# Performance work log

Hardware: AMD Instinct MI355X
Metric: run time of the kernel (lower is better)

The kernel has to match this reference:

```python
import jax, jax.numpy as jnp
import numpy as np

N = 100000   # nodes
E = 300000   # edges
D = 256      # emb_dim
FD = 512     # feat_dim
L = 5        # num_layer
G = 4000     # num graphs
NUM_ATOM = 100
NUM_BOND = 2
EPS = 1e-5


def setup_inputs() -> dict:
    key = jax.random.key(0)
    ks = jax.random.split(key, 24)
    s = 0.02
    inp = {
        "atomics": jax.random.randint(ks[0], (N,), 0, NUM_ATOM, dtype=jnp.int32),
        "pos": jax.random.normal(ks[1], (N, 3), dtype=jnp.float32),
        "edge_index": jax.random.randint(ks[2], (2, E), 0, N, dtype=jnp.int32),
        "edge_attr": jax.random.randint(ks[3], (E,), 0, NUM_BOND, dtype=jnp.int32),
        "batch": jnp.sort(jax.random.randint(ks[4], (N,), 0, G, dtype=jnp.int32)),
        # parameters
        "x_emb1": jax.random.normal(ks[5], (NUM_ATOM, D)) * s,
        "x_emb2_w": jax.random.normal(ks[6], (3, D)) * s,
        "x_emb2_b": jnp.zeros((D,), jnp.float32),
        "edge_emb": jax.random.normal(ks[7], (L, NUM_BOND, D)) * s,
        "mlp_w1": jax.random.normal(ks[8], (L, D, 2 * D)) * s,
        "mlp_b1": jnp.zeros((L, 2 * D), jnp.float32),
        "mlp_w2": jax.random.normal(ks[9], (L, 2 * D, D)) * s,
        "mlp_b2": jnp.zeros((L, D), jnp.float32),
        "bn_gamma": jnp.ones((L, D), jnp.float32),
        "bn_beta": jnp.zeros((L, D), jnp.float32),
        "feat_w": jax.random.normal(ks[10], (D, FD)) * s,
        "feat_b": jnp.zeros((FD,), jnp.float32),
        "head_w1": jax.random.normal(ks[11], (FD, FD // 2)) * s,
        "head_b1": jnp.zeros((FD // 2,), jnp.float32),
        "head_w2": jax.random.normal(ks[12], (FD // 2, 1)) * s,
        "head_b2": jnp.zeros((1,), jnp.float32),
    }
    return inp


def reference(atomics, pos, edge_index, edge_attr, batch,
              x_emb1, x_emb2_w, x_emb2_b, edge_emb,
              mlp_w1, mlp_b1, mlp_w2, mlp_b2, bn_gamma, bn_beta,
              feat_w, feat_b, head_w1, head_b1, head_w2, head_b2):
    n = atomics.shape[0]
    # initial node features: atom-type embedding + linear(pos)
    h = x_emb1[atomics] + pos @ x_emb2_w + x_emb2_b
    # add self loops (self-loop bond type = NUM_BOND-1)
    loop = jnp.arange(n, dtype=edge_index.dtype)
    src = jnp.concatenate([edge_index[0], loop])           # x_j (source)
    dst = jnp.concatenate([edge_index[1], loop])           # aggregate target
    eattr = jnp.concatenate([edge_attr,
                             jnp.full((n,), NUM_BOND - 1, dtype=edge_attr.dtype)])
    for l in range(L):
        msg = h[src] + edge_emb[l][eattr]                  # [E+N, D]
        agg = jax.ops.segment_sum(msg, dst, num_segments=n)
        # GINEConv MLP: Linear -> Softplus -> Linear
        h = jax.nn.softplus(agg @ mlp_w1[l] + mlp_b1[l]) @ mlp_w2[l] + mlp_b2[l]
        # BatchNorm1d (training mode: batch statistics, biased var)
        mean = h.mean(axis=0)
        var = h.var(axis=0)
        h = (h - mean) / jnp.sqrt(var + EPS) * bn_gamma[l] + bn_beta[l]
        if l < L - 1:
            h = jax.nn.softplus(h)
        # dropout with drop_ratio=0 is a no-op
    feat = h @ feat_w + feat_b                             # [N, FD]
    # global mean pool over graphs
    ssum = jax.ops.segment_sum(feat, batch, num_segments=G)
    cnt = jax.ops.segment_sum(jnp.ones((n,), feat.dtype), batch, num_segments=G)
    gfeat = ssum / jnp.maximum(cnt, 1.0)[:, None]          # [G, FD]
    hid = jax.nn.softplus(gfeat @ head_w1 + head_b1)
    return hid @ head_w2 + head_b2                          # [G, 1]
```

## Files before the change

kernel.cpp:

```cpp
#include <hip/hip_runtime.h>
#include <hip/hip_bf16.h>
#include <hip/hip_fp16.h>
#include <stdint.h>

#define D_  256
#define FD_ 512
#define L_  5
#define EPS_ 1e-5f

#define PLANE_SH 1056
#define TILE_SH  4224

typedef unsigned short ushort_t;
typedef __attribute__((ext_vector_type(8))) _Float16 h8v;
typedef __attribute__((ext_vector_type(4))) float    f4v;

__device__ __forceinline__ float sp(float x) {
    float t = __expf(-fabsf(x));
    return fmaxf(x, 0.f) + __logf(1.f + t);
}

__device__ __forceinline__ ushort_t f2h_bits(float v) {
    union { _Float16 h; ushort_t u; } c;
    c.h = (_Float16)v;
    return c.u;
}

__device__ __forceinline__ float h2f(ushort_t u) {
    union { ushort_t u; _Float16 h; } c;
    c.u = u;
    return (float)c.h;
}

__device__ __forceinline__ uint32_t pk2(float a, float b) {
    return (uint32_t)f2h_bits(a) | ((uint32_t)f2h_bits(b) << 16);
}

__device__ __forceinline__ size_t pk_off(int gm, int gn, int nKB) {
    return ((size_t)(gm >> 7) * nKB + (gn >> 5)) * TILE_SH
         + (size_t)((gn >> 3) & 3) * PLANE_SH
         + (gm & 127) * 8 + (gn & 7);
}

__global__ __launch_bounds__(256)
void init_h_kernel(const int* __restrict__ atomics, const float* __restrict__ pos,
                   const float* __restrict__ emb1, const float* __restrict__ w2,
                   const float* __restrict__ b2, ushort_t* __restrict__ h16, int N)
{
    int i = blockIdx.x;
    int d = threadIdx.x;
    int a = atomics[i];
    float p0 = pos[(size_t)i * 3 + 0];
    float p1 = pos[(size_t)i * 3 + 1];
    float p2 = pos[(size_t)i * 3 + 2];
    float v = emb1[(size_t)a * D_ + d]
            + p0 * w2[0 * D_ + d]
            + p1 * w2[1 * D_ + d]
            + p2 * w2[2 * D_ + d]
            + b2[d];
    h16[(size_t)i * D_ + d] = f2h_bits(v);
}

__global__ __launch_bounds__(256)
void hist_kernel(const int* __restrict__ dst, int* __restrict__ cnt, int E)
{
    int e = blockIdx.x * 256 + threadIdx.x;
    if (e < E) atomicAdd(&cnt[dst[e]], 1);
}

__global__ __launch_bounds__(256)
void alloc_kernel(const int* __restrict__ cnt, int* __restrict__ start,
                  int* __restrict__ cursor, int* __restrict__ total, int N)
{
    int i = blockIdx.x * 256 + threadIdx.x;
    if (i < N) {
        int s = atomicAdd(total, cnt[i]);
        start[i] = s;
        cursor[i] = s;
    }
}

__global__ __launch_bounds__(256)
void fill_kernel(const int* __restrict__ src, const int* __restrict__ dst,
                 const int* __restrict__ attr, int* __restrict__ cursor,
                 uint32_t* __restrict__ elist, int E)
{
    int e = blockIdx.x * 256 + threadIdx.x;
    if (e < E) {
        int p = atomicAdd(&cursor[dst[e]], 1);
        elist[p] = (uint32_t)src[e] | ((uint32_t)attr[e] << 30);
    }
}

__global__ __launch_bounds__(256)
void range_kernel(const int* __restrict__ batch, int* __restrict__ gstart,
                  int* __restrict__ gend, int N)
{
    int i = blockIdx.x * 256 + threadIdx.x;
    if (i >= N) return;
    int b = batch[i];
    if (i == 0 || batch[i - 1] != b) gstart[b] = i;
    if (i == N - 1 || batch[i + 1] != b) gend[b] = i + 1;
}

__global__ __launch_bounds__(256)
void act16_kernel(const ushort_t* __restrict__ h16, ushort_t* __restrict__ hact,
                  const float* __restrict__ bnsum, const float* __restrict__ gamma,
                  const float* __restrict__ beta, long long total16, float invN)
{
    __shared__ float ssc[256], ssh[256];
    int t = threadIdx.x;
    {
        float mean = bnsum[t] * invN;
        float var = bnsum[D_ + t] * invN - mean * mean;
        float sc = gamma[t] * rsqrtf(fmaxf(var, 0.f) + EPS_);
        ssc[t] = sc;
        ssh[t] = beta[t] - mean * sc;
    }
    __syncthreads();
    long long idx = (long long)blockIdx.x * 256 + t;
    if (idx >= total16) return;
    int c0 = (int)((idx * 16) & 255);
    uint4 in0 = *(const uint4*)(h16 + idx * 16);
    uint4 in1 = *(const uint4*)(h16 + idx * 16 + 8);
    ushort_t* ip0 = (ushort_t*)&in0;
    ushort_t* ip1 = (ushort_t*)&in1;
    ushort_t ov[16];
#pragma unroll
    for (int j = 0; j < 8; ++j)
        ov[j] = f2h_bits(sp(h2f(ip0[j]) * ssc[c0 + j] + ssh[c0 + j]));
#pragma unroll
    for (int j = 0; j < 8; ++j)
        ov[8 + j] = f2h_bits(sp(h2f(ip1[j]) * ssc[c0 + 8 + j] + ssh[c0 + 8 + j]));
    *(uint4*)(hact + idx * 16)     = *(uint4*)&ov[0];
    *(uint4*)(hact + idx * 16 + 8) = *(uint4*)&ov[8];
}

__global__ __launch_bounds__(256)
void gather2_kernel(const ushort_t* __restrict__ hact, const uint32_t* __restrict__ elist,
                    const int* __restrict__ start, const int* __restrict__ cnt,
                    const float* __restrict__ ee_l, ushort_t* __restrict__ aggP, int N)
{
    int t = threadIdx.x;
    int d0 = (t & 127) * 2;
    int ib = __builtin_amdgcn_readfirstlane(blockIdx.x * 8 + (t >> 7) * 4);
    float2 e0 = *(const float2*)(ee_l + d0);
    float2 e1 = *(const float2*)(ee_l + D_ + d0);
    int sbase[4], sdeg[4];
    float ax[4], ay[4];
    int mdeg = 0;
#pragma unroll
    for (int r = 0; r < 4; ++r) {
        int i = ib + r;
        sbase[r] = 0; sdeg[r] = 0; ax[r] = 0.f; ay[r] = 0.f;
        if (i < N) {
            sbase[r] = start[i];
            sdeg[r]  = cnt[i];
            uint32_t hv = *(const uint32_t*)(hact + (size_t)i * D_ + d0);
            ax[r] = h2f((ushort_t)hv) + e1.x;
            ay[r] = h2f((ushort_t)(hv >> 16)) + e1.y;
            mdeg = (sdeg[r] > mdeg) ? sdeg[r] : mdeg;
        }
    }
    for (int j = 0; j < mdeg; j += 2) {
        uint32_t pA[4], pB[4];
#pragma unroll
        for (int r = 0; r < 4; ++r) {
            pA[r] = elist[(j     < sdeg[r]) ? sbase[r] + j     : 0];
            pB[r] = elist[(j + 1 < sdeg[r]) ? sbase[r] + j + 1 : 0];
        }
        uint32_t hvA[4], hvB[4];
#pragma unroll
        for (int r = 0; r < 4; ++r)
            hvA[r] = *(const uint32_t*)(hact + (size_t)(pA[r] & 0x3FFFFFFF) * D_ + d0);
#pragma unroll
        for (int r = 0; r < 4; ++r)
            hvB[r] = *(const uint32_t*)(hact + (size_t)(pB[r] & 0x3FFFFFFF) * D_ + d0);
#pragma unroll
        for (int r = 0; r < 4; ++r) {
            if (j < sdeg[r]) {
                bool b1 = (pA[r] >> 30) != 0;
                ax[r] += h2f((ushort_t)hvA[r]) + (b1 ? e1.x : e0.x);
                ay[r] += h2f((ushort_t)(hvA[r] >> 16)) + (b1 ? e1.y : e0.y);
            }
            if (j + 1 < sdeg[r]) {
                bool b1 = (pB[r] >> 30) != 0;
                ax[r] += h2f((ushort_t)hvB[r]) + (b1 ? e1.x : e0.x);
                ay[r] += h2f((ushort_t)(hvB[r] >> 16)) + (b1 ? e1.y : e0.y);
            }
        }
    }
#pragma unroll
    for (int r = 0; r < 4; ++r) {
        int i = ib + r;
        if (i < N) {
            size_t o = pk_off(i, d0, 8);
            *(uint32_t*)(aggP + o) = pk2(ax[r], ay[r]);
        }
    }
}

__global__ __launch_bounds__(256)
void pool_bn_kernel(const ushort_t* __restrict__ h16, const float* __restrict__ bnsum,
                    const float* __restrict__ gamma, const float* __restrict__ beta,
                    const int* __restrict__ gstart, const int* __restrict__ gend,
                    ushort_t* __restrict__ poolP, float invN)
{
    int g = blockIdx.x;
    int d = threadIdx.x;
    float mean = bnsum[d] * invN;
    float var = bnsum[D_ + d] * invN - mean * mean;
    float sc = gamma[d] * rsqrtf(fmaxf(var, 0.f) + EPS_);
    float sh = beta[d] - mean * sc;
    int s0 = gstart[g], s1 = gend[g];
    float acc = 0.f;
    int i = s0;
    for (; i + 4 <= s1; i += 4) {
        float a0 = h2f(h16[(size_t)(i + 0) * D_ + d]);
        float a1 = h2f(h16[(size_t)(i + 1) * D_ + d]);
        float a2 = h2f(h16[(size_t)(i + 2) * D_ + d]);
        float a3 = h2f(h16[(size_t)(i + 3) * D_ + d]);
        acc += (a0 + a1) + (a2 + a3);
    }
    for (; i < s1; ++i)
        acc += h2f(h16[(size_t)i * D_ + d]);
    int cnt = s1 - s0;
    float mval = (cnt > 0) ? (sc * acc / (float)cnt + sh) : 0.f;
    poolP[pk_off(g, d, 8)] = f2h_bits(mval);
}

__global__ __launch_bounds__(256)
void convert_w_pack(const float* __restrict__ W, ushort_t* __restrict__ dh,
                    int N, int nKB)
{
    int kb = blockIdx.x, nb = blockIdx.y;
    int n = threadIdx.x >> 1, half = threadIdx.x & 1;
#pragma unroll
    for (int j = 0; j < 2; ++j) {
        int kq = half * 2 + j;
        size_t o = (size_t)(nb * nKB + kb) * TILE_SH + kq * PLANE_SH + n * 8;
#pragma unroll
        for (int jj = 0; jj < 8; ++jj) {
            float w = W[(size_t)(kb * 32 + kq * 8 + jj) * N + nb * 128 + n];
            dh[o + jj] = f2h_bits(w);
        }
    }
}

__global__ __launch_bounds__(512, 4)
void fused_mlp_kernel(const ushort_t* __restrict__ APK,
                      const ushort_t* __restrict__ W1P,
                      const ushort_t* __restrict__ W2P,
                      const float* __restrict__ b1,
                      const float* __restrict__ b2,
                      ushort_t* __restrict__ Hout,
                      float* __restrict__ bnsum,
                      int m)
{
    __shared__ ushort_t Tl[32768];

    int rb = blockIdx.x;
    int tid = threadIdx.x, w = tid >> 6, lane = tid & 63;
    int fr = lane & 15, kq = lane >> 4;

    const ushort_t* aT = APK + (size_t)(rb >> 1) * (8 * TILE_SH)
                       + (size_t)kq * PLANE_SH + (size_t)((rb & 1) * 64 + fr) * 8;
    const ushort_t* bT = W1P + (size_t)(w >> 1) * (8 * TILE_SH)
                       + (size_t)kq * PLANE_SH + (size_t)((w & 1) * 64 + fr) * 8;

    f4v acc1[4][4];
#pragma unroll
    for (int i = 0; i < 4; ++i)
#pragma unroll
        for (int j = 0; j < 4; ++j)
            acc1[i][j] = (f4v){0.f, 0.f, 0.f, 0.f};

    for (int kb = 0; kb < 8; ++kb) {
        h8v Af[4], Wf[4];
#pragma unroll
        for (int t = 0; t < 4; ++t) {
            Af[t] = *(const h8v*)(aT + (size_t)kb * TILE_SH + t * 128);
            Wf[t] = *(const h8v*)(bT + (size_t)kb * TILE_SH + t * 128);
        }
        __builtin_amdgcn_s_setprio(1);
#pragma unroll
        for (int nt = 0; nt < 4; ++nt)
#pragma unroll
            for (int mt = 0; mt < 4; ++mt)
                acc1[nt][mt] = __builtin_amdgcn_mfma_f32_16x16x32_f16(
                    Wf[nt], Af[mt], acc1[nt][mt], 0, 0, 0);
        __builtin_amdgcn_s_setprio(0);
    }

#pragma unroll
    for (int nt = 0; nt < 4; ++nt) {
        float4 b1v = *(const float4*)(b1 + w * 64 + nt * 16 + kq * 4);
        int baseu = (w * 2 + (nt >> 1)) * 2048
                  + ((nt & 1) * 2 + (kq >> 1)) * 512
                  + (kq & 1) * 4;
#pragma unroll
        for (int mt = 0; mt < 4; ++mt) {
            uint2 val;
            val.x = pk2(sp(acc1[nt][mt][0] + b1v.x), sp(acc1[nt][mt][1] + b1v.y));
            val.y = pk2(sp(acc1[nt][mt][2] + b1v.z), sp(acc1[nt][mt][3] + b1v.w));
            *(uint2*)(Tl + baseu + (mt * 16 + fr) * 8) = val;
        }
    }
    __syncthreads();

    const ushort_t* wT = W2P + (size_t)(w >> 2) * (16 * TILE_SH)
                       + (size_t)kq * PLANE_SH + (size_t)((w & 3) * 32 + fr) * 8;

    f4v acc2[4][2];
#pragma unroll
    for (int i = 0; i < 4; ++i)
#pragma unroll
        for (int j = 0; j < 2; ++j)
            acc2[i][j] = (f4v){0.f, 0.f, 0.f, 0.f};

    for (int kb = 0; kb < 16; ++kb) {
        h8v Tf[4], Wf[2];
#pragma unroll
        for (int t = 0; t < 4; ++t)
            Tf[t] = *(const h8v*)(Tl + kb * 2048 + kq * 512 + (fr + t * 16) * 8);
#pragma unroll
        for (int t = 0; t < 2; ++t)
            Wf[t] = *(const h8v*)(wT + (size_t)kb * TILE_SH + t * 128);
        __builtin_amdgcn_s_setprio(1);
#pragma unroll
        for (int rt = 0; rt < 4; ++rt)
#pragma unroll
            for (int ct = 0; ct < 2; ++ct)
                acc2[rt][ct] = __builtin_amdgcn_mfma_f32_16x16x32_f16(
                    Tf[rt], Wf[ct], acc2[rt][ct], 0, 0, 0);
        __builtin_amdgcn_s_setprio(0);
    }

    int gm0 = rb * 64 + kq * 4;
#pragma unroll
    for (int ct = 0; ct < 2; ++ct) {
        int gn = w * 32 + ct * 16 + fr;
        float bv = b2[gn];
        float s = 0.f, ss = 0.f;
#pragma unroll
        for (int rt = 0; rt < 4; ++rt)
#pragma unroll
            for (int rr = 0; rr < 4; ++rr) {
                int gm = gm0 + rt * 16 + rr;
                if (gm < m) {
                    float v = acc2[rt][ct][rr] + bv;
                    Hout[(size_t)gm * D_ + gn] = f2h_bits(v);
                    s += v;
                    ss += v * v;
                }
            }
        s  += __shfl_xor(s, 16);  s  += __shfl_xor(s, 32);
        ss += __shfl_xor(ss, 16); ss += __shfl_xor(ss, 32);
        if (kq == 0) {
            atomicAdd(&bnsum[gn], s);
            atomicAdd(&bnsum[D_ + gn], ss);
        }
    }
}

template <int EPI>
__global__ __launch_bounds__(256, 3)
void gemm_p16(const ushort_t* __restrict__ APK, const ushort_t* __restrict__ BPK,
              const float* __restrict__ bias,
              ushort_t* __restrict__ Tout, float* __restrict__ Cout,
              float* __restrict__ bnsum, const int* __restrict__ batch,
              int m, int N, int nKB)
{
    const int NB = N >> 7;
    const int mb = (m + 127) >> 7;
    int id = blockIdx.x;
    int grp = id / (8 * NB);
    int rem = id - grp * 8 * NB;
    int nb = rem >> 3;
    int rb = grp * 8 + (rem & 7);
    if (rb >= mb) return;

    int tid = threadIdx.x, wave = tid >> 6, lane = tid & 63;
    int wr = wave >> 1, wc = wave & 1;
    int fr = lane & 15, kq = lane >> 4;

    const ushort_t* aP = APK + (size_t)rb * nKB * TILE_SH
                       + (size_t)kq * PLANE_SH + (size_t)(wr * 64 + fr) * 8;
    const ushort_t* bP = BPK + (size_t)nb * nKB * TILE_SH
                       + (size_t)kq * PLANE_SH + (size_t)(wc * 64 + fr) * 8;

    f4v acc[4][4];
#pragma unroll
    for (int i = 0; i < 4; ++i)
#pragma unroll
        for (int j = 0; j < 4; ++j)
            acc[i][j] = (f4v){0.f, 0.f, 0.f, 0.f};

    h8v Fa[4], Fb[4], Ga[4], Gb[4];

#define LOADF(dA, dB, kbi)                                                   \
    {   const ushort_t* ap_ = aP + (size_t)(kbi) * TILE_SH;                  \
        const ushort_t* bp_ = bP + (size_t)(kbi) * TILE_SH;                  \
        _Pragma("unroll")                                                    \
        for (int t = 0; t < 4; ++t) {                                        \
            dA[t] = *(const h8v*)(ap_ + t * 128);                            \
            dB[t] = *(const h8v*)(bp_ + t * 128);                            \
        } }

#define MFMA16(sA, sB)                                                       \
    {   __builtin_amdgcn_s_setprio(1);                                       \
        _Pragma("unroll")                                                    \
        for (int rt = 0; rt < 4; ++rt)                                       \
            _Pragma("unroll")                                                \
            for (int ct = 0; ct < 4; ++ct)                                   \
                acc[rt][ct] = __builtin_amdgcn_mfma_f32_16x16x32_f16(        \
                    sA[rt], sB[ct], acc[rt][ct], 0, 0, 0);                   \
        __builtin_amdgcn_s_setprio(0); }

    LOADF(Fa, Fb, 0);
    for (int kb = 0; kb < nKB; kb += 2) {
        LOADF(Ga, Gb, kb + 1);
        MFMA16(Fa, Fb);
        if (kb + 2 < nKB) LOADF(Fa, Fb, kb + 2);
        MFMA16(Ga, Gb);
    }
#undef LOADF
#undef MFMA16

    int gm00 = rb * 128 + wr * 64 + kq * 4;
    int gn0  = nb * 128 + wc * 64 + fr;
    int nKBo = N >> 5;
    size_t tileRow = (size_t)(rb * nKBo + nb * 4 + wc * 2) * TILE_SH
                   + (size_t)((wr * 64 + kq * 4) * 8 + (fr & 7));
#pragma unroll
    for (int ct = 0; ct < 4; ++ct) {
        int gn = gn0 + ct * 16;
        float bv = bias[gn];
        float s = 0.f, ss = 0.f;
        size_t cb = tileRow + (size_t)(ct >> 1) * TILE_SH
                  + (size_t)((2 * ct + (fr >> 3)) & 3) * PLANE_SH;
#pragma unroll
        for (int rt = 0; rt < 4; ++rt) {
            if (EPI == 2) {
                int bp = -1; float run = 0.f;
#pragma unroll
                for (int rr = 0; rr < 4; ++rr) {
                    int gm = gm00 + rt * 16 + rr;
                    if (gm >= m) continue;
                    float v = acc[rt][ct][rr] + bv;
                    int bg = batch[gm];
                    if (bg == bp) { run += v; }
                    else {
                        if (bp >= 0) atomicAdd(&Cout[(size_t)bp * N + gn], run);
                        bp = bg; run = v;
                    }
                }
                if (bp >= 0) atomicAdd(&Cout[(size_t)bp * N + gn], run);
            } else {
#pragma unroll
                for (int rr = 0; rr < 4; ++rr) {
                    int gm = gm00 + rt * 16 + rr;
                    if (gm >= m) continue;
                    float v = acc[rt][ct][rr] + bv;
                    if (EPI == 0) {
                        Tout[cb + (rt * 16 + rr) * 8] = f2h_bits(sp(v));
                    } else if (EPI == 1) {
                        Tout[(size_t)gm * N + gn] = f2h_bits(v);
                        s += v;
                        ss += v * v;
                    } else {
                        Cout[(size_t)gm * N + gn] = v;
                    }
                }
            }
        }
        if (EPI == 1) {
            s  += __shfl_xor(s, 16);  s  += __shfl_xor(s, 32);
            ss += __shfl_xor(ss, 16); ss += __shfl_xor(ss, 32);
            if (kq == 0) {
                atomicAdd(&bnsum[gn], s);
                atomicAdd(&bnsum[D_ + gn], ss);
            }
        }
    }
}

#define BM 64
#define BN 64
#define BK 16

__global__ __launch_bounds__(256)
void gemm_head(const float* __restrict__ A, const float* __restrict__ W,
               const float* __restrict__ bias, float* __restrict__ C,
               int M, int N, int K)
{
    __shared__ float As[BK][BM + 4];
    __shared__ float Ws[BK][BN + 4];

    int tid = threadIdx.x;
    int bm = blockIdx.y * BM;
    int bn = blockIdx.x * BN;
    int tx = tid & 15;
    int ty = tid >> 4;

    float acc[4][4] = {};

    int a_m = tid >> 2;
    int a_k = (tid & 3) * 4;
    int w_k = tid >> 4;
    int w_n = (tid & 15) * 4;

    for (int k0 = 0; k0 < K; k0 += BK) {
        int gm = bm + a_m;
        float4 av = make_float4(0.f, 0.f, 0.f, 0.f);
        if (gm < M)
            av = *(const float4*)(A + (size_t)gm * K + k0 + a_k);
        As[a_k + 0][a_m] = av.x;
        As[a_k + 1][a_m] = av.y;
        As[a_k + 2][a_m] = av.z;
        As[a_k + 3][a_m] = av.w;

        float4 wv = *(const float4*)(W + (size_t)(k0 + w_k) * N + bn + w_n);
        *(float4*)&Ws[w_k][w_n] = wv;

        __syncthreads();

#pragma unroll
        for (int k = 0; k < BK; ++k) {
            float4 a4 = *(const float4*)&As[k][ty * 4];
            float4 b4 = *(const float4*)&Ws[k][tx * 4];
            float a[4] = {a4.x, a4.y, a4.z, a4.w};
            float b[4] = {b4.x, b4.y, b4.z, b4.w};
#pragma unroll
            for (int i = 0; i < 4; ++i)
#pragma unroll
                for (int j = 0; j < 4; ++j)
                    acc[i][j] += a[i] * b[j];
        }
        __syncthreads();
    }

#pragma unroll
    for (int i = 0; i < 4; ++i) {
        int gm = bm + ty * 4 + i;
        if (gm >= M) continue;
#pragma unroll
        for (int j = 0; j < 4; ++j) {
            int gn = bn + tx * 4 + j;
            C[(size_t)gm * N + gn] = sp(acc[i][j] + bias[gn]);
        }
    }
}

__global__ __launch_bounds__(256)
void head2_kernel(const float* __restrict__ hid, const float* __restrict__ w2,
                  const float* __restrict__ b2, float* __restrict__ out, int G)
{
    __shared__ float red[256];
    int g = blockIdx.x;
    int t = threadIdx.x;
    float v = hid[(size_t)g * 256 + t] * w2[t];
    red[t] = v;
    __syncthreads();
    for (int s = 128; s > 0; s >>= 1) {
        if (t < s) red[t] += red[t + s];
        __syncthreads();
    }
    if (t == 0) out[g] = red[0] + b2[0];
}

extern "C" void kernel_launch(void* const* d_in, const int* in_sizes, int n_in,
                              void* d_out, int out_size, void* d_ws, size_t ws_size,
                              hipStream_t stream)
{
    const int N = in_sizes[0];
    const int E = in_sizes[3];
    const int G = out_size;

    const int*   atomics  = (const int*)d_in[0];
    const float* pos      = (const float*)d_in[1];
    const int*   eidx     = (const int*)d_in[2];
    const int*   eattr    = (const int*)d_in[3];
    const int*   batch    = (const int*)d_in[4];
    const float* x_emb1   = (const float*)d_in[5];
    const float* x_emb2_w = (const float*)d_in[6];
    const float* x_emb2_b = (const float*)d_in[7];
    const float* edge_emb = (const float*)d_in[8];
    const float* mlp_w1   = (const float*)d_in[9];
    const float* mlp_b1   = (const float*)d_in[10];
    const float* mlp_w2   = (const float*)d_in[11];
    const float* mlp_b2   = (const float*)d_in[12];
    const float* bn_g     = (const float*)d_in[13];
    const float* bn_b     = (const float*)d_in[14];
    const float* feat_w   = (const float*)d_in[15];
    const float* feat_b   = (const float*)d_in[16];
    const float* head_w1  = (const float*)d_in[17];
    const float* head_b1  = (const float*)d_in[18];
    const float* head_w2  = (const float*)d_in[19];
    const float* head_b2  = (const float*)d_in[20];
    float* out = (float*)d_out;

    const int* src = eidx;
    const int* dst = eidx + E;

    char* ws = (char*)d_ws;
    size_t off = 0;
    auto carve = [&](size_t bytes) {
        void* p = ws + off;
        off += (bytes + 255) & ~(size_t)255;
        return p;
    };

    const int nRB = (N + 127) / 128;
    const int nGB = (G + 127) / 128;

    ushort_t* h16  = (ushort_t*)carve((size_t)N * D_ * 2);
    ushort_t* hact = (ushort_t*)carve((size_t)N * D_ * 2);
    ushort_t* aggP = (ushort_t*)carve((size_t)nRB * 8 * TILE_SH * 2);
    const size_t WTILES = 32 * TILE_SH;
    ushort_t* w1P = (ushort_t*)carve((size_t)L_ * WTILES * 2);
    ushort_t* w2P = (ushort_t*)carve((size_t)L_ * WTILES * 2);
    ushort_t* fP  = (ushort_t*)carve(WTILES * 2);
    float* bnsum  = (float*)carve(2 * D_ * 4);
    float* gfeat  = (float*)carve((size_t)G * FD_ * 4);
    float* hid    = (float*)carve((size_t)G * (FD_ / 2) * 4);
    ushort_t* poolP = (ushort_t*)carve((size_t)nGB * 8 * TILE_SH * 2);
    int* gstart  = (int*)carve((size_t)G * 4);
    int* gend    = (int*)carve((size_t)G * 4);
    int* cnt_i   = (int*)carve((size_t)N * 4);
    int* start_i = (int*)carve((size_t)N * 4);
    int* cursor  = (int*)carve((size_t)N * 4);
    int* total   = (int*)carve(4);
    uint32_t* elist = (uint32_t*)carve((size_t)E * 4);

    const float invN = 1.f / (float)N;

    hipMemsetAsync(cnt_i, 0, (size_t)N * 4, stream);
    hipMemsetAsync(total, 0, 4, stream);
    hipMemsetAsync(gstart, 0, (size_t)G * 4, stream);
    hipMemsetAsync(gend, 0, (size_t)G * 4, stream);
    hist_kernel<<<(E + 255) / 256, 256, 0, stream>>>(dst, cnt_i, E);
    alloc_kernel<<<(N + 255) / 256, 256, 0, stream>>>(cnt_i, start_i, cursor, total, N);
    fill_kernel<<<(E + 255) / 256, 256, 0, stream>>>(src, dst, eattr, cursor, elist, E);
    range_kernel<<<(N + 255) / 256, 256, 0, stream>>>(batch, gstart, gend, N);

    for (int l = 0; l < L_; ++l) {
        convert_w_pack<<<dim3(8, 4), 256, 0, stream>>>(
            mlp_w1 + (size_t)l * D_ * FD_, w1P + (size_t)l * WTILES, FD_, 8);
        convert_w_pack<<<dim3(16, 2), 256, 0, stream>>>(
            mlp_w2 + (size_t)l * FD_ * D_, w2P + (size_t)l * WTILES, D_, 16);
    }
    convert_w_pack<<<dim3(8, 4), 256, 0, stream>>>(feat_w, fP, FD_, 8);

    init_h_kernel<<<N, 256, 0, stream>>>(atomics, pos, x_emb1, x_emb2_w, x_emb2_b, h16, N);

    const long long total16 = (long long)N * D_ / 16;
    const int ACTB = (int)((total16 + 255) / 256);
    const int GB8 = (N + 7) / 8;
    const int FB  = (N + 63) / 64;

    for (int l = 0; l < L_; ++l) {
        const float* ee_l = edge_emb + (size_t)l * 2 * D_;
        const ushort_t* gsrc = h16;
        if (l > 0) {
            act16_kernel<<<ACTB, 256, 0, stream>>>(h16, hact, bnsum,
                bn_g + (size_t)(l - 1) * D_, bn_b + (size_t)(l - 1) * D_,
                total16, invN);
            gsrc = hact;
        }
        gather2_kernel<<<GB8, 256, 0, stream>>>(gsrc, elist, start_i, cnt_i,
                                                ee_l, aggP, N);

        hipMemsetAsync(bnsum, 0, 2 * D_ * 4, stream);
        fused_mlp_kernel<<<FB, 512, 0, stream>>>(
            aggP, w1P + (size_t)l * WTILES, w2P + (size_t)l * WTILES,
            mlp_b1 + (size_t)l * FD_, mlp_b2 + (size_t)l * D_,
            h16, bnsum, N);
    }

    pool_bn_kernel<<<G, 256, 0, stream>>>(h16, bnsum, bn_g + (size_t)(L_ - 1) * D_,
                                          bn_b + (size_t)(L_ - 1) * D_,
                                          gstart, gend, poolP, invN);
    auto swgrid = [](int mb, int NBc) { return ((mb + 7) / 8) * 8 * NBc; };
    gemm_p16<3><<<swgrid(nGB, 4), 256, 0, stream>>>(
        poolP, fP, feat_b, nullptr, gfeat, nullptr, nullptr, G, FD_, 8);

    gemm_head<<<dim3((FD_ / 2) / BN, (G + BM - 1) / BM), 256, 0, stream>>>(
        gfeat, head_w1, head_b1, hid, G, FD_ / 2, FD_);
    head2_kernel<<<G, 256, 0, stream>>>(hid, head_w2, head_b2, out, G);
}
```

Baseline: 1.156 ms.

## Stage A tile in LDS via direct global-to-LDS loads and split hidden dim in halves

The fused MLP kernel now copies the block's 64-row A tile into shared memory once, using global_load_lds, instead of having every wave re-read it from global memory. The first GEMM's 512-wide hidden dimension is processed in two 256-wide halves, each immediately consumed by the second GEMM. This halves the intermediate LDS buffer and the acc1 register footprint, which may help occupancy. The cost is extra barriers per block and a less overlapped schedule between the two phases.

```diff
diff --git a/kernel.cpp b/kernel.cpp
--- a/kernel.cpp
+++ b/kernel.cpp
@@ -34,6 +34,12 @@
 
 __device__ __forceinline__ uint32_t pk2(float a, float b) {
     return (uint32_t)f2h_bits(a) | ((uint32_t)f2h_bits(b) << 16);
+}
+
+__device__ __forceinline__ void gload_lds16(const void* g, void* l) {
+    __builtin_amdgcn_global_load_lds((const __attribute__((address_space(1))) void*)g,
+                                     (__attribute__((address_space(3))) void*)l,
+                                     16, 0, 0);
 }
 
 __device__ __forceinline__ size_t pk_off(int gm, int gn, int nKB) {
@@ -257,83 +263,103 @@
                       float* __restrict__ bnsum,
                       int m)
 {
-    __shared__ ushort_t Tl[32768];
+    __shared__ ushort_t Al[16384];
+    __shared__ ushort_t Tl[16384];
 
     int rb = blockIdx.x;
     int tid = threadIdx.x, w = tid >> 6, lane = tid & 63;
     int fr = lane & 15, kq = lane >> 4;
 
-    const ushort_t* aT = APK + (size_t)(rb >> 1) * (8 * TILE_SH)
-                       + (size_t)kq * PLANE_SH + (size_t)((rb & 1) * 64 + fr) * 8;
-    const ushort_t* bT = W1P + (size_t)(w >> 1) * (8 * TILE_SH)
-                       + (size_t)kq * PLANE_SH + (size_t)((w & 1) * 64 + fr) * 8;
-
-    f4v acc1[4][4];
+    {
+        const ushort_t* aBase = APK + (size_t)(rb >> 1) * (8 * TILE_SH)
+                              + (size_t)(rb & 1) * 64 * 8;
+#pragma unroll
+        for (int j = 0; j < 4; ++j) {
+            int c = w * 4 + j;
+            int kb = c >> 2, p = c & 3;
+            const ushort_t* g = aBase + (size_t)kb * TILE_SH
+                              + (size_t)p * PLANE_SH + (size_t)lane * 8;
+            gload_lds16(g, Al + kb * 2048 + p * 512);
+        }
+    }
+
+    f4v acc2[4][2];
 #pragma unroll
     for (int i = 0; i < 4; ++i)
 #pragma unroll
-        for (int j = 0; j < 4; ++j)
-            acc1[i][j] = (f4v){0.f, 0.f, 0.f, 0.f};
-
-    for (int kb = 0; kb < 8; ++kb) {
-        h8v Af[4], Wf[4];
-#pragma unroll
-        for (int t = 0; t < 4; ++t) {
-            Af[t] = *(const h8v*)(aT + (size_t)kb * TILE_SH + t * 128);
-            Wf[t] = *(const h8v*)(bT + (size_t)kb * TILE_SH + t * 128);
-        }
-        __builtin_amdgcn_s_setprio(1);
-#pragma unroll
-        for (int nt = 0; nt < 4; ++nt)
-#pragma unroll
-            for (int mt = 0; mt < 4; ++mt)
-                acc1[nt][mt] = __builtin_amdgcn_mfma_f32_16x16x32_f16(
-                    Wf[nt], Af[mt], acc1[nt][mt], 0, 0, 0);
-        __builtin_amdgcn_s_setprio(0);
-    }
-
-#pragma unroll
-    for (int nt = 0; nt < 4; ++nt) {
-        float4 b1v = *(const float4*)(b1 + w * 64 + nt * 16 + kq * 4);
-        int baseu = (w * 2 + (nt >> 1)) * 2048
-                  + ((nt & 1) * 2 + (kq >> 1)) * 512
-                  + (kq & 1) * 4;
-#pragma unroll
-        for (int mt = 0; mt < 4; ++mt) {
-            uint2 val;
-            val.x = pk2(sp(acc1[nt][mt][0] + b1v.x), sp(acc1[nt][mt][1] + b1v.y));
-            val.y = pk2(sp(acc1[nt][mt][2] + b1v.z), sp(acc1[nt][mt][3] + b1v.w));
-            *(uint2*)(Tl + baseu + (mt * 16 + fr) * 8) = val;
-        }
-    }
+        for (int j = 0; j < 2; ++j)
+            acc2[i][j] = (f4v){0.f, 0.f, 0.f, 0.f};
+
+    asm volatile("s_waitcnt vmcnt(0)" ::: "memory");
     __syncthreads();
 
     const ushort_t* wT = W2P + (size_t)(w >> 2) * (16 * TILE_SH)
                        + (size_t)kq * PLANE_SH + (size_t)((w & 3) * 32 + fr) * 8;
 
-    f4v acc2[4][2];
-#pragma unroll
-    for (int i = 0; i < 4; ++i)
-#pragma unroll
-        for (int j = 0; j < 2; ++j)
-            acc2[i][j] = (f4v){0.f, 0.f, 0.f, 0.f};
-
-    for (int kb = 0; kb < 16; ++kb) {
-        h8v Tf[4], Wf[2];
-#pragma unroll
-        for (int t = 0; t < 4; ++t)
-            Tf[t] = *(const h8v*)(Tl + kb * 2048 + kq * 512 + (fr + t * 16) * 8);
-#pragma unroll
-        for (int t = 0; t < 2; ++t)
-            Wf[t] = *(const h8v*)(wT + (size_t)kb * TILE_SH + t * 128);
-        __builtin_amdgcn_s_setprio(1);
-#pragma unroll
-        for (int rt = 0; rt < 4; ++rt)
-#pragma unroll
-            for (int ct = 0; ct < 2; ++ct)
-                acc2[rt][ct] = __builtin_amdgcn_mfma_f32_16x16x32_f16(
-                    Tf[rt], Wf[ct], acc2[rt][ct], 0, 0, 0);
-        __builtin_amdgcn_s_setprio(0);
+#pragma unroll
+    for (int hh = 0; hh < 2; ++hh) {
+        const ushort_t* bT = W1P + (size_t)(hh * 2 + (w >> 2)) * (8 * TILE_SH)
+                           + (size_t)kq * PLANE_SH
+                           + (size_t)((w & 3) * 32 + fr) * 8;
+
+        f4v acc1[2][4];
+#pragma unroll
+        for (int i = 0; i < 2; ++i)
+#pragma unroll
+            for (int j = 0; j < 4; ++j)
+                acc1[i][j] = (f4v){0.f, 0.f, 0.f, 0.f};
+
+        for (int kb = 0; kb < 8; ++kb) {
+            h8v Af[4], Wf[2];
+#pragma unroll
+            for (int t = 0; t < 4; ++t)
+                Af[t] = *(const h8v*)(Al + kb * 2048 + kq * 512 + (t * 16 + fr) * 8);
+#pragma unroll
+            for (int t = 0; t < 2; ++t)
+                Wf[t] = *(const h8v*)(bT + (size_t)kb * TILE_SH + t * 128);
+            __builtin_amdgcn_s_setprio(1);
+#pragma unroll
+            for (int nt = 0; nt < 2; ++nt)
+#pragma unroll
+                for (int mt = 0; mt < 4; ++mt)
+                    acc1[nt][mt] = __builtin_amdgcn_mfma_f32_16x16x32_f16(
+                        Wf[nt], Af[mt], acc1[nt][mt], 0, 0, 0);
+            __builtin_amdgcn_s_setprio(0);
+        }
+
+        if (hh == 1) __syncthreads();
+
+#pragma unroll
+        for (int nt = 0; nt < 2; ++nt) {
+            float4 b1v = *(const float4*)(b1 + hh * 256 + w * 32 + nt * 16 + kq * 4);
+            int baseu = w * 2048 + (nt * 2 + (kq >> 1)) * 512 + (kq & 1) * 4;
+#pragma unroll
+            for (int mt = 0; mt < 4; ++mt) {
+                uint2 val;
+                val.x = pk2(sp(acc1[nt][mt][0] + b1v.x), sp(acc1[nt][mt][1] + b1v.y));
+                val.y = pk2(sp(acc1[nt][mt][2] + b1v.z), sp(acc1[nt][mt][3] + b1v.w));
+                *(uint2*)(Tl + baseu + (mt * 16 + fr) * 8) = val;
+            }
+        }
+        __syncthreads();
+
+        for (int kb = 0; kb < 8; ++kb) {
+            h8v Tf[4], Wf[2];
+#pragma unroll
+            for (int t = 0; t < 4; ++t)
+                Tf[t] = *(const h8v*)(Tl + kb * 2048 + kq * 512 + (fr + t * 16) * 8);
+#pragma unroll
+            for (int t = 0; t < 2; ++t)
+                Wf[t] = *(const h8v*)(wT + (size_t)(hh * 8 + kb) * TILE_SH + t * 128);
+            __builtin_amdgcn_s_setprio(1);
+#pragma unroll
+            for (int rt = 0; rt < 4; ++rt)
+#pragma unroll
+                for (int ct = 0; ct < 2; ++ct)
+                    acc2[rt][ct] = __builtin_amdgcn_mfma_f32_16x16x32_f16(
+                        Tf[rt], Wf[ct], acc2[rt][ct], 0, 0, 0);
+            __builtin_amdgcn_s_setprio(0);
+        }
     }
 
     int gm0 = rb * 64 + kq * 4;
```

After: 1.174 ms. Within noise of the previous version (+1.5%).
